# Kernel tuning notes

Hardware: AMD Instinct MI355X
Metric: run time of the kernel (lower is better)

## Reference

```python
import jax, jax.numpy as jnp
import numpy as np

D_MODEL = 512
D_INNER = 1024   # expand * d_model
D_STATE = 16
D_CONV = 4
DT_RANK = 32     # ceil(d_model / 16)
N_LAYERS = 4
N_PRED_LAYERS = 2
FEAT = 128
LN_EPS = 1e-5


def _ln(x, w, b):
    m = x.mean(-1, keepdims=True)
    v = ((x - m) ** 2).mean(-1, keepdims=True)
    return (x - m) * jax.lax.rsqrt(v + LN_EPS) * w + b


def _silu(x):
    return x * jax.nn.sigmoid(x)


def _causal_conv(x, w, b):
    # depthwise causal conv1d: x (B,L,C), w (C,K), b (C,)
    K = w.shape[1]
    L = x.shape[1]
    xp = jnp.pad(x, ((0, 0), (K - 1, 0), (0, 0)))
    y = b
    for k in range(K):
        y = y + xp[:, k:k + L, :] * w[:, k]
    return y


def _mamba(x, in_w, conv_w, conv_b, xp_w, dt_w, dt_b, Alog, Dp, out_w):
    # x: (B,L,d_model)
    xz = jnp.einsum('bld,ed->ble', x, in_w)          # (B,L,2*d_inner)
    xi, z = jnp.split(xz, 2, axis=-1)
    xc = _silu(_causal_conv(xi, conv_w, conv_b))     # (B,L,d_inner)
    dbc = jnp.einsum('blc,ec->ble', xc, xp_w)        # (B,L,dt_rank+2N)
    dt = dbc[..., :DT_RANK]
    Bm = dbc[..., DT_RANK:DT_RANK + D_STATE]         # (B,L,N)
    Cm = dbc[..., DT_RANK + D_STATE:]                # (B,L,N)
    delta = jax.nn.softplus(jnp.einsum('blr,cr->blc', dt, dt_w) + dt_b)  # (B,L,d_inner)
    A = -jnp.exp(Alog)                               # (d_inner,N), negative
    dA = jnp.exp(delta[..., None] * A)               # (B,L,d_inner,N)
    dBu = delta[..., None] * Bm[:, :, None, :] * xc[..., None]

    def step(h, inp):
        dA_t, dBu_t, C_t = inp
        h = dA_t * h + dBu_t                         # (B,d_inner,N)
        y = jnp.einsum('bcn,bn->bc', h, C_t)
        return h, y

    h0 = jnp.zeros((x.shape[0], D_INNER, D_STATE), x.dtype)
    _, ys = jax.lax.scan(step, h0, (dA.transpose(1, 0, 2, 3),
                                    dBu.transpose(1, 0, 2, 3),
                                    Cm.transpose(1, 0, 2)))
    y = ys.transpose(1, 0, 2) + Dp * xc              # skip connection D*u
    y = y * _silu(z)
    return jnp.einsum('blc,dc->bld', y, out_w)


def _forward(x, inp_w, inp_b, enc_ln_w, enc_ln_b, enc_in_w, enc_conv_w, enc_conv_b,
             enc_xp_w, enc_dt_w, enc_dt_b, enc_Alog, enc_D, enc_out_w,
             fin_ln_w, fin_ln_b, prd_ln_w, prd_ln_b, prd_in_w, prd_conv_w, prd_conv_b,
             prd_xp_w, prd_dt_w, prd_dt_b, prd_Alog, prd_D, prd_out_w,
             prd_nrm_w, prd_nrm_b, prd_proj_w, prd_proj_b):
    # MambaEncoder: input_proj + n_layers pre-norm residual Mamba blocks + final LN
    h = jnp.einsum('blf,df->bld', x, inp_w) + inp_b
    for i in range(N_LAYERS):
        h = h + _mamba(_ln(h, enc_ln_w[i], enc_ln_b[i]),
                       enc_in_w[i], enc_conv_w[i], enc_conv_b[i], enc_xp_w[i],
                       enc_dt_w[i], enc_dt_b[i], enc_Alog[i], enc_D[i], enc_out_w[i])
    ctx = _ln(h, fin_ln_w, fin_ln_b)
    # MambaPredictor: small causal mamba stack + norm + proj
    p = ctx
    for i in range(N_PRED_LAYERS):
        p = p + _mamba(_ln(p, prd_ln_w[i], prd_ln_b[i]),
                       prd_in_w[i], prd_conv_w[i], prd_conv_b[i], prd_xp_w[i],
                       prd_dt_w[i], prd_dt_b[i], prd_Alog[i], prd_D[i], prd_out_w[i])
    p = _ln(p, prd_nrm_w, prd_nrm_b)
    preds = jnp.einsum('bld,ed->ble', p, prd_proj_w) + prd_proj_b
    return preds


def _mamba_params(key, n, scale=0.02):
    ks = jax.random.split(key, 6)
    arange_A = jnp.tile(jnp.log(jnp.arange(1, D_STATE + 1, dtype=jnp.float32)), (n, D_INNER, 1))
    return dict(
        in_w=jax.random.normal(ks[0], (n, 2 * D_INNER, D_MODEL)) * scale,
        conv_w=jax.random.normal(ks[1], (n, D_INNER, D_CONV)) * scale,
        conv_b=jnp.zeros((n, D_INNER)),
        xp_w=jax.random.normal(ks[2], (n, DT_RANK + 2 * D_STATE, D_INNER)) * scale,
        dt_w=jax.random.normal(ks[3], (n, D_INNER, DT_RANK)) * scale,
        dt_b=jnp.full((n, D_INNER), jnp.log(jnp.expm1(0.01))),  # inv-softplus(0.01)
        Alog=arange_A,
        D=jnp.ones((n, D_INNER)),
        out_w=jax.random.normal(ks[4], (n, D_MODEL, D_INNER)) * scale,
    )


def setup_inputs() -> dict:
    key = jax.random.key(0)
    ks = jax.random.split(key, 8)
    enc = _mamba_params(ks[0], N_LAYERS)
    prd = _mamba_params(ks[1], N_PRED_LAYERS)
    return {
        'x': jax.random.normal(ks[2], (2, 1024, FEAT), dtype=jnp.float32),
        'inp_w': jax.random.normal(ks[3], (D_MODEL, FEAT)) * 0.02,
        'inp_b': jnp.zeros((D_MODEL,)),
        'enc_ln_w': jnp.ones((N_LAYERS, D_MODEL)), 'enc_ln_b': jnp.zeros((N_LAYERS, D_MODEL)),
        'enc_in_w': enc['in_w'], 'enc_conv_w': enc['conv_w'], 'enc_conv_b': enc['conv_b'],
        'enc_xp_w': enc['xp_w'], 'enc_dt_w': enc['dt_w'], 'enc_dt_b': enc['dt_b'],
        'enc_Alog': enc['Alog'], 'enc_D': enc['D'], 'enc_out_w': enc['out_w'],
        'fin_ln_w': jnp.ones((D_MODEL,)), 'fin_ln_b': jnp.zeros((D_MODEL,)),
        'prd_ln_w': jnp.ones((N_PRED_LAYERS, D_MODEL)), 'prd_ln_b': jnp.zeros((N_PRED_LAYERS, D_MODEL)),
        'prd_in_w': prd['in_w'], 'prd_conv_w': prd['conv_w'], 'prd_conv_b': prd['conv_b'],
        'prd_xp_w': prd['xp_w'], 'prd_dt_w': prd['dt_w'], 'prd_dt_b': prd['dt_b'],
        'prd_Alog': prd['Alog'], 'prd_D': prd['D'], 'prd_out_w': prd['out_w'],
        'prd_nrm_w': jnp.ones((D_MODEL,)), 'prd_nrm_b': jnp.zeros((D_MODEL,)),
        'prd_proj_w': jax.random.normal(ks[4], (D_MODEL, D_MODEL)) * 0.02,
        'prd_proj_b': jnp.zeros((D_MODEL,)),
    }


def reference(x, inp_w, inp_b, enc_ln_w, enc_ln_b, enc_in_w, enc_conv_w, enc_conv_b,
              enc_xp_w, enc_dt_w, enc_dt_b, enc_Alog, enc_D, enc_out_w,
              fin_ln_w, fin_ln_b, prd_ln_w, prd_ln_b, prd_in_w, prd_conv_w, prd_conv_b,
              prd_xp_w, prd_dt_w, prd_dt_b, prd_Alog, prd_D, prd_out_w,
              prd_nrm_w, prd_nrm_b, prd_proj_w, prd_proj_b):
    return _forward(x, inp_w, inp_b, enc_ln_w, enc_ln_b, enc_in_w, enc_conv_w, enc_conv_b,
                    enc_xp_w, enc_dt_w, enc_dt_b, enc_Alog, enc_D, enc_out_w,
                    fin_ln_w, fin_ln_b, prd_ln_w, prd_ln_b, prd_in_w, prd_conv_w, prd_conv_b,
                    prd_xp_w, prd_dt_w, prd_dt_b, prd_Alog, prd_D, prd_out_w,
                    prd_nrm_w, prd_nrm_b, prd_proj_w, prd_proj_b)
```

## Files before the change

kernel.cpp:

```cpp
#include <hip/hip_runtime.h>
#include <hip/hip_bf16.h>

using bf16 = __hip_bfloat16;
typedef __attribute__((ext_vector_type(8))) short short8;
typedef __attribute__((ext_vector_type(4))) float f32x4;

static constexpr int LB = 2;
static constexpr int LL = 1024;
static constexpr int DM = 512;
static constexpr int DI = 1024;
static constexpr int DSN = 16;
static constexpr int RK = 32;
static constexpr int MR_ROWS = LB * LL;

static constexpr int NCHUNK = 64;
static constexpr int CH = LL / NCHUNK;

__device__ __forceinline__ void gload16(const void* g, void* l) {
    __builtin_amdgcn_global_load_lds(
        (__attribute__((address_space(1))) void*)(g),
        (__attribute__((address_space(3))) void*)(l), 16, 0, 0);
}

struct ConvArgs {
    const float* src[9];
    bf16*        dst[9];
    int          n4[9];
};

__global__ __launch_bounds__(256) void convert_bf16_multi(ConvArgs a) {
    const int s = blockIdx.y;
    const float4* __restrict__ src = (const float4*)a.src[s];
    bf16* __restrict__ dst = a.dst[s];
    const int n4 = a.n4[s];
    for (int i = blockIdx.x * 256 + threadIdx.x; i < n4; i += gridDim.x * 256) {
        float4 v = src[i];
        bf16 t[4] = {__float2bfloat16(v.x), __float2bfloat16(v.y),
                     __float2bfloat16(v.z), __float2bfloat16(v.w)};
        *(uint2*)(dst + (size_t)i * 4) = *(uint2*)t;
    }
}

__global__ __launch_bounds__(256) void transpose_dtw(const float* __restrict__ enc_dtw,
                                                     const float* __restrict__ prd_dtw,
                                                     float* __restrict__ out) {
    const int layer = blockIdx.y;
    const float* src = (layer < 4) ? enc_dtw + (size_t)layer * DI * RK
                                   : prd_dtw + (size_t)(layer - 4) * DI * RK;
    float* dst = out + (size_t)layer * RK * DI;
    const int idx = blockIdx.x * 256 + threadIdx.x;
    const int k = idx >> 10, c = idx & (DI - 1);
    dst[idx] = src[(size_t)c * RK + k];
}

__device__ __forceinline__ void ln_store8(float* outrow, int lane,
                                          const float* v) {
    float4 a = {v[0], v[1], v[2], v[3]}, b = {v[4], v[5], v[6], v[7]};
    ((float4*)outrow)[lane] = a;
    ((float4*)outrow)[lane + 64] = b;
}
__device__ __forceinline__ void ln_store8(bf16* outrow, int lane,
                                          const float* v) {
    bf16 t0[4] = {__float2bfloat16(v[0]), __float2bfloat16(v[1]),
                  __float2bfloat16(v[2]), __float2bfloat16(v[3])};
    bf16 t1[4] = {__float2bfloat16(v[4]), __float2bfloat16(v[5]),
                  __float2bfloat16(v[6]), __float2bfloat16(v[7])};
    ((uint2*)outrow)[lane] = *(uint2*)t0;
    ((uint2*)outrow)[lane + 64] = *(uint2*)t1;
}

template <typename T>
__global__ __launch_bounds__(256) void ln_kernel(const float* __restrict__ x,
                                                 const float* __restrict__ w,
                                                 const float* __restrict__ b,
                                                 T* __restrict__ out,
                                                 float* __restrict__ dbc_zero) {
    if (dbc_zero != nullptr && blockIdx.x < 128) {
        ((float4*)dbc_zero)[blockIdx.x * 256 + threadIdx.x] =
            make_float4(0.f, 0.f, 0.f, 0.f);
    }
    const int wid = threadIdx.x >> 6, lane = threadIdx.x & 63;
    const int row = blockIdx.x * 4 + wid;
    const float4* xr = (const float4*)(x + (size_t)row * DM);
    const float4 v0 = xr[lane], v1 = xr[lane + 64];

    float s = (v0.x + v0.y + v0.z + v0.w) + (v1.x + v1.y + v1.z + v1.w);
#pragma unroll
    for (int m = 1; m < 64; m <<= 1) s += __shfl_xor(s, m);
    const float mean = s * (1.f / DM);

    float d[8] = {v0.x - mean, v0.y - mean, v0.z - mean, v0.w - mean,
                  v1.x - mean, v1.y - mean, v1.z - mean, v1.w - mean};
    float s2 = 0.f;
#pragma unroll
    for (int q = 0; q < 8; ++q) s2 += d[q] * d[q];
#pragma unroll
    for (int m = 1; m < 64; m <<= 1) s2 += __shfl_xor(s2, m);
    const float rs = rsqrtf(s2 * (1.f / DM) + 1e-5f);

    const float4 w0 = ((const float4*)w)[lane], w1 = ((const float4*)w)[lane + 64];
    const float4 b0 = ((const float4*)b)[lane], b1 = ((const float4*)b)[lane + 64];
    float o[8] = {d[0] * rs * w0.x + b0.x, d[1] * rs * w0.y + b0.y,
                  d[2] * rs * w0.z + b0.z, d[3] * rs * w0.w + b0.w,
                  d[4] * rs * w1.x + b1.x, d[5] * rs * w1.y + b1.y,
                  d[6] * rs * w1.z + b1.z, d[7] * rs * w1.w + b1.w};
    ln_store8(out + (size_t)row * DM, lane, o);
}

template <int BM, int BN, int BK, int EPI>
__global__ __launch_bounds__(256) void gemm_bt(const bf16* __restrict__ A, int lda,
                                               const bf16* __restrict__ B, int ldb,
                                               float* __restrict__ C, int ldc,
                                               int K, const float* __restrict__ bias) {
    static_assert(BK == 64, "layout assumes 128B LDS row");
    static_assert(BM % 32 == 0 && BN % 32 == 0, "wave staging granularity");
    constexpr int MR = (BM / 2) / 16;
    constexpr int NR = (BN / 2) / 16;
    __shared__ __align__(16) char sA[BM * 128];
    __shared__ __align__(16) char sB[BN * 128];

    const int tid = threadIdx.x;
    const int lane = tid & 63, wid = tid >> 6;
    const int wr = wid >> 1, wc = wid & 1;
    const int m0 = blockIdx.y * BM, n0 = blockIdx.x * BN;
    const int kbase = (EPI == 2) ? blockIdx.z * K : 0;

    f32x4 acc[MR][NR] = {};

    const int lrow = lane >> 3;
    const int lcol = (lane & 7) ^ lrow;
    const size_t lda2 = (size_t)lda * 2, ldb2 = (size_t)ldb * 2;
    const char* Ab = (const char*)A + (size_t)(m0 + wid * (BM / 4) + lrow) * lda2
                     + lcol * 16 + (size_t)kbase * 2;
    const char* Bb = (const char*)B + (size_t)(n0 + wid * (BN / 4) + lrow) * ldb2
                     + lcol * 16 + (size_t)kbase * 2;
    char* sAw = sA + wid * (BM / 4) * 128;
    char* sBw = sB + wid * (BN / 4) * 128;

    for (int k0 = 0; k0 < K; k0 += BK) {
#pragma unroll
        for (int i = 0; i < BM / 32; ++i)
            gload16(Ab + (size_t)i * 8 * lda2 + (size_t)k0 * 2, sAw + i * 1024);
#pragma unroll
        for (int i = 0; i < BN / 32; ++i)
            gload16(Bb + (size_t)i * 8 * ldb2 + (size_t)k0 * 2, sBw + i * 1024);
        __syncthreads();
#pragma unroll
        for (int kk = 0; kk < BK; kk += 32) {
            const int kb2 = (kk + (lane >> 4) * 8) * 2;
            short8 af[MR], bfr[NR];
#pragma unroll
            for (int m = 0; m < MR; ++m) {
                const int r = wr * (BM / 2) + m * 16 + (lane & 15);
                af[m] = *(const short8*)(sA + r * 128 + (kb2 ^ ((r & 7) << 4)));
            }
#pragma unroll
            for (int n = 0; n < NR; ++n) {
                const int r = wc * (BN / 2) + n * 16 + (lane & 15);
                bfr[n] = *(const short8*)(sB + r * 128 + (kb2 ^ ((r & 7) << 4)));
            }
#pragma unroll
            for (int m = 0; m < MR; ++m) {
#pragma unroll
                for (int n = 0; n < NR; ++n) {
                    acc[m][n] = __builtin_amdgcn_mfma_f32_16x16x32_bf16(af[m], bfr[n], acc[m][n], 0, 0, 0);
                }
            }
        }
        __syncthreads();
    }

#pragma unroll
    for (int m = 0; m < MR; ++m) {
#pragma unroll
        for (int n = 0; n < NR; ++n) {
            const int col = n0 + wc * (BN / 2) + n * 16 + (lane & 15);
            const float bv = (EPI == 1) ? bias[col] : 0.f;
#pragma unroll
            for (int j = 0; j < 4; ++j) {
                const int row = m0 + wr * (BM / 2) + m * 16 + (lane >> 4) * 4 + j;
                float v = acc[m][n][j] + bv;
                if (EPI == 4) {
                    ((bf16*)C)[(size_t)row * ldc + col] = __float2bfloat16(v);
                } else {
                    float* p = C + (size_t)row * ldc + col;
                    if (EPI == 2) {
                        atomicAdd(p, v);
                    } else {
                        if (EPI == 3) v += *p;
                        *p = v;
                    }
                }
            }
        }
    }
}

__global__ __launch_bounds__(256) void conv_mfma(const bf16* __restrict__ xzb,
                                                 const float* __restrict__ cw,
                                                 const float* __restrict__ cb,
                                                 const bf16* __restrict__ xpw,
                                                 bf16* __restrict__ xc_bf,
                                                 float* __restrict__ dbc) {
    const int c0 = blockIdx.x * 64;
    const int r0 = blockIdx.y * 64;
    const int tid = threadIdx.x, lane = tid & 63, wid = tid >> 6;
    __shared__ __align__(16) char sX[64 * 128];
    __shared__ __align__(16) char sW[64 * 128];

    const int lrow = lane >> 3, lcol = (lane & 7) ^ lrow;
    {
        const char* Wb = (const char*)xpw + (size_t)(wid * 16 + lrow) * (DI * 2)
                         + c0 * 2 + lcol * 16;
        char* sWw = sW + wid * 16 * 128;
        gload16(Wb, sWw);
        gload16(Wb + 8 * (DI * 2), sWw + 8 * 128);
    }

    const int c = lane;
    const int rgrp = wid;
    const float4 w = *(const float4*)(cw + (size_t)(c0 + c) * 4);
    const float cbv = cb[c0 + c];
#pragma unroll
    for (int i = 0; i < 16; ++i) {
        const int r = rgrp + i * 4;
        const int rowg = r0 + r;
        const int bstart = (rowg >> 10) << 10;
        const bf16* xi = xzb + (size_t)rowg * (2 * DI) + c0 + c;
        float acc = cbv + w.w * __bfloat162float(xi[0]);
        if (rowg - 1 >= bstart) acc += w.z * __bfloat162float(xi[-(2 * DI)]);
        if (rowg - 2 >= bstart) acc += w.y * __bfloat162float(xi[-(4 * DI)]);
        if (rowg - 3 >= bstart) acc += w.x * __bfloat162float(xi[-(6 * DI)]);
        const float s = acc / (1.f + expf(-acc));
        const bf16 sb = __float2bfloat16(s);
        xc_bf[(size_t)rowg * DI + c0 + c] = sb;
        *(bf16*)(sX + r * 128 + ((c * 2) ^ ((r & 7) << 4))) = sb;
    }
    __syncthreads();

    f32x4 acc[4] = {};
    const int kb2 = (lane >> 4) * 16;
#pragma unroll
    for (int kk = 0; kk < 2; ++kk) {
        const int kbyte = kk * 64 + kb2;
        const int ra = wid * 16 + (lane & 15);
        const short8 af = *(const short8*)(sX + ra * 128 + (kbyte ^ ((ra & 7) << 4)));
#pragma unroll
        for (int n = 0; n < 4; ++n) {
            const int re = n * 16 + (lane & 15);
            const short8 bfr = *(const short8*)(sW + re * 128 + (kbyte ^ ((re & 7) << 4)));
            acc[n] = __builtin_amdgcn_mfma_f32_16x16x32_bf16(af, bfr, acc[n], 0, 0, 0);
        }
    }
#pragma unroll
    for (int n = 0; n < 4; ++n) {
        const int col = n * 16 + (lane & 15);
#pragma unroll
        for (int j = 0; j < 4; ++j) {
            const int row = r0 + wid * 16 + (lane >> 4) * 4 + j;
            atomicAdd(&dbc[(size_t)row * 64 + col], acc[n][j]);
        }
    }
}

__global__ __launch_bounds__(256) void scan_part1(const bf16* __restrict__ xcb,
                                                  const float* __restrict__ dbc,
                                                  const float* __restrict__ Alog,
                                                  const float* __restrict__ dtw_t,
                                                  const float* __restrict__ dtb,
                                                  float* __restrict__ psum,
                                                  float* __restrict__ ssum) {
    const int lane = threadIdx.x & 63;
    const int wsub = threadIdx.x >> 6;
    const int c = blockIdx.x * 64 + lane;
    const int chunk = blockIdx.y * 4 + wsub;
    const int b = blockIdx.z;
    const int r0 = b * LL + chunk * CH;

    float wv[RK];
#pragma unroll
    for (int k = 0; k < RK; ++k) wv[k] = dtw_t[(size_t)k * DI + c];
    const float bdt = dtb[c];

    float a2[DSN];
#pragma unroll
    for (int q = 0; q < 4; ++q) {
        const float4 al = *(const float4*)(Alog + (size_t)c * DSN + q * 4);
        a2[q * 4 + 0] = -expf(al.x) * 1.44269504f;
        a2[q * 4 + 1] = -expf(al.y) * 1.44269504f;
        a2[q * 4 + 2] = -expf(al.z) * 1.44269504f;
        a2[q * 4 + 3] = -expf(al.w) * 1.44269504f;
    }

    float h[DSN], P[DSN];
#pragma unroll
    for (int n = 0; n < DSN; ++n) { h[n] = 0.f; P[n] = 1.f; }

    for (int t = 0; t < CH; ++t) {
        const size_t r = r0 + t;
        float acc = bdt;
#pragma unroll
        for (int q = 0; q < RK / 4; ++q) {
            const float4 d4 = *(const float4*)(dbc + r * 64 + q * 4);
            acc = fmaf(d4.x, wv[q * 4 + 0], acc);
            acc = fmaf(d4.y, wv[q * 4 + 1], acc);
            acc = fmaf(d4.z, wv[q * 4 + 2], acc);
            acc = fmaf(d4.w, wv[q * 4 + 3], acc);
        }
        const float d = (acc > 20.f) ? acc : log1pf(expf(acc));

        const float xv = __bfloat162float(xcb[r * DI + c]);
        const float dxv = d * xv;
        float Bv[DSN];
#pragma unroll
        for (int q = 0; q < 4; ++q)
            *(float4*)&Bv[q * 4] = *(const float4*)(dbc + r * 64 + 32 + q * 4);
#pragma unroll
        for (int n = 0; n < DSN; ++n) {
            const float dA = exp2f(d * a2[n]);
            h[n] = fmaf(dA, h[n], dxv * Bv[n]);
            P[n] *= dA;
        }
    }

    const size_t obase = ((size_t)(b * NCHUNK + chunk) * DSN) * DI + c;
#pragma unroll
    for (int n = 0; n < DSN; ++n) {
        psum[obase + (size_t)n * DI] = P[n];
        ssum[obase + (size_t)n * DI] = h[n];
    }
}

__global__ __launch_bounds__(256) void scan_combine(float* __restrict__ psum,
                                                    const float* __restrict__ ssum) {
    const int lane = threadIdx.x & 63;
    const int idx = blockIdx.y * 4 + (threadIdx.x >> 6);
    const int b = idx >> 4, n = idx & 15;
    const int c = blockIdx.x * 64 + lane;
    const size_t base = ((size_t)(b * NCHUNK) * DSN + n) * DI + c;
    const size_t stride = (size_t)DSN * DI;

    float h = 0.f;
    for (int j0 = 0; j0 < NCHUNK; j0 += 8) {
        float Pv[8], Sv[8];
#pragma unroll
        for (int u = 0; u < 8; ++u) {
            Pv[u] = psum[base + (j0 + u) * stride];
            Sv[u] = ssum[base + (j0 + u) * stride];
        }
#pragma unroll
        for (int u = 0; u < 8; ++u) {
            psum[base + (j0 + u) * stride] = h;
            h = fmaf(Pv[u], h, Sv[u]);
        }
    }
}

__global__ __launch_bounds__(256) void scan_part3(const bf16* __restrict__ xcb,
                                                  const bf16* __restrict__ xzb,
                                                  const float* __restrict__ dbc,
                                                  const float* __restrict__ Alog,
                                                  const float* __restrict__ dtw_t,
                                                  const float* __restrict__ dtb,
                                                  const float* __restrict__ Dp,
                                                  const float* __restrict__ hin,
                                                  bf16* __restrict__ yg) {
    const int lane = threadIdx.x & 63;
    const int wsub = threadIdx.x >> 6;
    const int c = blockIdx.x * 64 + lane;
    const int chunk = blockIdx.y * 4 + wsub;
    const int b = blockIdx.z;
    const int r0 = b * LL + chunk * CH;

    float wv[RK];
#pragma unroll
    for (int k = 0; k < RK; ++k) wv[k] = dtw_t[(size_t)k * DI + c];
    const float bdt = dtb[c];

    float a2[DSN];
#pragma unroll
    for (int q = 0; q < 4; ++q) {
        const float4 al = *(const float4*)(Alog + (size_t)c * DSN + q * 4);
        a2[q * 4 + 0] = -expf(al.x) * 1.44269504f;
        a2[q * 4 + 1] = -expf(al.y) * 1.44269504f;
        a2[q * 4 + 2] = -expf(al.z) * 1.44269504f;
        a2[q * 4 + 3] = -expf(al.w) * 1.44269504f;
    }
    const float dp = Dp[c];

    float h[DSN];
    const size_t hbase = ((size_t)(b * NCHUNK + chunk) * DSN) * DI + c;
#pragma unroll
    for (int n = 0; n < DSN; ++n) h[n] = hin[hbase + (size_t)n * DI];

    for (int t = 0; t < CH; ++t) {
        const size_t r = r0 + t;
        float acc = bdt;
#pragma unroll
        for (int q = 0; q < RK / 4; ++q) {
            const float4 d4 = *(const float4*)(dbc + r * 64 + q * 4);
            acc = fmaf(d4.x, wv[q * 4 + 0], acc);
            acc = fmaf(d4.y, wv[q * 4 + 1], acc);
            acc = fmaf(d4.z, wv[q * 4 + 2], acc);
            acc = fmaf(d4.w, wv[q * 4 + 3], acc);
        }
        const float d = (acc > 20.f) ? acc : log1pf(expf(acc));

        const float xv = __bfloat162float(xcb[r * DI + c]);
        const float zv = __bfloat162float(xzb[r * (2 * DI) + DI + c]);
        const float dxv = d * xv;
        float Bv[DSN], Cv[DSN];
#pragma unroll
        for (int q = 0; q < 4; ++q) {
            *(float4*)&Bv[q * 4] = *(const float4*)(dbc + r * 64 + 32 + q * 4);
            *(float4*)&Cv[q * 4] = *(const float4*)(dbc + r * 64 + 48 + q * 4);
        }
        float y0 = 0.f, y1 = 0.f, y2 = 0.f, y3 = 0.f;
#pragma unroll
        for (int q = 0; q < 4; ++q) {
            {
                const float dA = exp2f(d * a2[q * 4 + 0]);
                h[q * 4 + 0] = fmaf(dA, h[q * 4 + 0], dxv * Bv[q * 4 + 0]);
                y0 = fmaf(h[q * 4 + 0], Cv[q * 4 + 0], y0);
            }
            {
                const float dA = exp2f(d * a2[q * 4 + 1]);
                h[q * 4 + 1] = fmaf(dA, h[q * 4 + 1], dxv * Bv[q * 4 + 1]);
                y1 = fmaf(h[q * 4 + 1], Cv[q * 4 + 1], y1);
            }
            {
                const float dA = exp2f(d * a2[q * 4 + 2]);
                h[q * 4 + 2] = fmaf(dA, h[q * 4 + 2], dxv * Bv[q * 4 + 2]);
                y2 = fmaf(h[q * 4 + 2], Cv[q * 4 + 2], y2);
            }
            {
                const float dA = exp2f(d * a2[q * 4 + 3]);
                h[q * 4 + 3] = fmaf(dA, h[q * 4 + 3], dxv * Bv[q * 4 + 3]);
                y3 = fmaf(h[q * 4 + 3], Cv[q * 4 + 3], y3);
            }
        }
        const float y = (y0 + y1) + (y2 + y3);
        const float zs = zv / (1.f + expf(-zv));
        yg[r * DI + c] = __float2bfloat16((y + dp * xv) * zs);
    }
}

static void run_mamba_layer(hipStream_t stream, float* resid,
                            const float* ln_w, const float* ln_b,
                            const bf16* inw_bf,
                            const float* conv_w, const float* conv_b,
                            const bf16* xpw_bf,
                            const float* dtw_t, const float* dt_b,
                            const float* Alog, const float* Dp,
                            const bf16* outw_bf,
                            bf16* ln_bf, bf16* xzb, bf16* xc_bf,
                            float* dbc,
                            float* psum, float* ssum, bf16* yg_bf) {
    ln_kernel<bf16><<<MR_ROWS / 4, 256, 0, stream>>>(resid, ln_w, ln_b, ln_bf, dbc);
    gemm_bt<64, 64, 64, 4><<<dim3(2 * DI / 64, MR_ROWS / 64), 256, 0, stream>>>(
        ln_bf, DM, inw_bf, DM, (float*)xzb, 2 * DI, DM, nullptr);
    conv_mfma<<<dim3(DI / 64, MR_ROWS / 64), 256, 0, stream>>>(
        xzb, conv_w, conv_b, xpw_bf, xc_bf, dbc);
    scan_part1<<<dim3(DI / 64, NCHUNK / 4, LB), 256, 0, stream>>>(
        xc_bf, dbc, Alog, dtw_t, dt_b, psum, ssum);
    scan_combine<<<dim3(DI / 64, (LB * DSN) / 4), 256, 0, stream>>>(psum, ssum);
    scan_part3<<<dim3(DI / 64, NCHUNK / 4, LB), 256, 0, stream>>>(
        xc_bf, xzb, dbc, Alog, dtw_t, dt_b, Dp, psum, yg_bf);
    gemm_bt<32, 64, 64, 3><<<dim3(DM / 64, MR_ROWS / 32), 256, 0, stream>>>(
        yg_bf, DI, outw_bf, DI, resid, DM, DI, nullptr);
}

extern "C" void kernel_launch(void* const* d_in, const int* in_sizes, int n_in,
                              void* d_out, int out_size, void* d_ws, size_t ws_size,
                              hipStream_t stream) {
    const float* x         = (const float*)d_in[0];
    const float* inp_w     = (const float*)d_in[1];
    const float* inp_b     = (const float*)d_in[2];
    const float* enc_ln_w  = (const float*)d_in[3];
    const float* enc_ln_b  = (const float*)d_in[4];
    const float* enc_in_w  = (const float*)d_in[5];
    const float* enc_conv_w= (const float*)d_in[6];
    const float* enc_conv_b= (const float*)d_in[7];
    const float* enc_xp_w  = (const float*)d_in[8];
    const float* enc_dt_w  = (const float*)d_in[9];
    const float* enc_dt_b  = (const float*)d_in[10];
    const float* enc_Alog  = (const float*)d_in[11];
    const float* enc_D     = (const float*)d_in[12];
    const float* enc_out_w = (const float*)d_in[13];
    const float* fin_ln_w  = (const float*)d_in[14];
    const float* fin_ln_b  = (const float*)d_in[15];
    const float* prd_ln_w  = (const float*)d_in[16];
    const float* prd_ln_b  = (const float*)d_in[17];
    const float* prd_in_w  = (const float*)d_in[18];
    const float* prd_conv_w= (const float*)d_in[19];
    const float* prd_conv_b= (const float*)d_in[20];
    const float* prd_xp_w  = (const float*)d_in[21];
    const float* prd_dt_w  = (const float*)d_in[22];
    const float* prd_dt_b  = (const float*)d_in[23];
    const float* prd_Alog  = (const float*)d_in[24];
    const float* prd_D     = (const float*)d_in[25];
    const float* prd_out_w = (const float*)d_in[26];
    const float* prd_nrm_w = (const float*)d_in[27];
    const float* prd_nrm_b = (const float*)d_in[28];
    const float* prd_proj_w= (const float*)d_in[29];
    const float* prd_proj_b= (const float*)d_in[30];

    char* wp = (char*)d_ws;
    auto carve = [&](size_t elems, size_t esz) {
        void* p = (void*)wp;
        wp += (elems * esz + 255) & ~(size_t)255;
        return p;
    };
    bf16* x_bf     = (bf16*)carve((size_t)MR_ROWS * 128, 2);
    bf16* inpw_bf  = (bf16*)carve((size_t)DM * 128, 2);
    bf16* einw_bf  = (bf16*)carve(4ull * 2 * DI * DM, 2);
    bf16* expw_bf  = (bf16*)carve(4ull * 64 * DI, 2);
    bf16* eoutw_bf = (bf16*)carve(4ull * DM * DI, 2);
    bf16* pinw_bf  = (bf16*)carve(2ull * 2 * DI * DM, 2);
    bf16* pxpw_bf  = (bf16*)carve(2ull * 64 * DI, 2);
    bf16* poutw_bf = (bf16*)carve(2ull * DM * DI, 2);
    bf16* projw_bf = (bf16*)carve((size_t)DM * DM, 2);
    float* dtwt    = (float*)carve(6ull * RK * DI, 4);
    float* hbuf    = (float*)carve((size_t)MR_ROWS * DM, 4);
    float* pbuf    = (float*)carve((size_t)MR_ROWS * DM, 4);
    bf16* ln_bf    = (bf16*)carve((size_t)MR_ROWS * DM, 2);
    bf16* xzb      = (bf16*)carve((size_t)MR_ROWS * 2 * DI, 2);
    bf16* xc_bf    = (bf16*)carve((size_t)MR_ROWS * DI, 2);
    float* dbc     = (float*)carve((size_t)MR_ROWS * 64, 4);
    float* psum    = (float*)carve((size_t)LB * NCHUNK * DSN * DI, 4);
    float* ssum    = (float*)carve((size_t)LB * NCHUNK * DSN * DI, 4);
    bf16* yg_bf    = (bf16*)carve((size_t)MR_ROWS * DI, 2);

    ConvArgs ca;
    const float* csrc[9] = {x, inp_w, enc_in_w, enc_xp_w, enc_out_w,
                            prd_in_w, prd_xp_w, prd_out_w, prd_proj_w};
    bf16* cdst[9] = {x_bf, inpw_bf, einw_bf, expw_bf, eoutw_bf,
                     pinw_bf, pxpw_bf, poutw_bf, projw_bf};
    const int cn[9] = {MR_ROWS * 128, DM * 128, 4 * 2 * DI * DM, 4 * 64 * DI, 4 * DM * DI,
                       2 * 2 * DI * DM, 2 * 64 * DI, 2 * DM * DI, DM * DM};
    for (int i = 0; i < 9; ++i) { ca.src[i] = csrc[i]; ca.dst[i] = cdst[i]; ca.n4[i] = cn[i] / 4; }
    convert_bf16_multi<<<dim3(128, 9), 256, 0, stream>>>(ca);
    transpose_dtw<<<dim3(RK * DI / 256, 6), 256, 0, stream>>>(enc_dt_w, prd_dt_w, dtwt);

    gemm_bt<32, 64, 64, 1><<<dim3(DM / 64, MR_ROWS / 32), 256, 0, stream>>>(
        x_bf, 128, inpw_bf, 128, hbuf, DM, 128, inp_b);

    for (int i = 0; i < 4; ++i) {
        run_mamba_layer(stream, hbuf,
                        enc_ln_w + (size_t)i * DM, enc_ln_b + (size_t)i * DM,
                        einw_bf + (size_t)i * 2 * DI * DM,
                        enc_conv_w + (size_t)i * DI * 4, enc_conv_b + (size_t)i * DI,
                        expw_bf + (size_t)i * 64 * DI,
                        dtwt + (size_t)i * RK * DI, enc_dt_b + (size_t)i * DI,
                        enc_Alog + (size_t)i * DI * DSN, enc_D + (size_t)i * DI,
                        eoutw_bf + (size_t)i * DM * DI,
                        ln_bf, xzb, xc_bf, dbc, psum, ssum, yg_bf);
    }

    ln_kernel<float><<<MR_ROWS / 4, 256, 0, stream>>>(hbuf, fin_ln_w, fin_ln_b, pbuf, nullptr);

    for (int i = 0; i < 2; ++i) {
        run_mamba_layer(stream, pbuf,
                        prd_ln_w + (size_t)i * DM, prd_ln_b + (size_t)i * DM,
                        pinw_bf + (size_t)i * 2 * DI * DM,
                        prd_conv_w + (size_t)i * DI * 4, prd_conv_b + (size_t)i * DI,
                        pxpw_bf + (size_t)i * 64 * DI,
                        dtwt + (size_t)(4 + i) * RK * DI, prd_dt_b + (size_t)i * DI,
                        prd_Alog + (size_t)i * DI * DSN, prd_D + (size_t)i * DI,
                        poutw_bf + (size_t)i * DM * DI,
                        ln_bf, xzb, xc_bf, dbc, psum, ssum, yg_bf);
    }

    ln_kernel<bf16><<<MR_ROWS / 4, 256, 0, stream>>>(pbuf, prd_nrm_w, prd_nrm_b, ln_bf, nullptr);
    gemm_bt<32, 64, 64, 1><<<dim3(DM / 64, MR_ROWS / 32), 256, 0, stream>>>(
        ln_bf, DM, projw_bf, DM, (float*)d_out, DM, DM, prd_proj_b);

    (void)in_sizes; (void)n_in; (void)out_size; (void)ws_size;
}
```

Measured before the change: 693.7 us.

## Fuse LayerNorm into in-proj GEMM and split conv from x-proj GEMM

Adds a new ln_gemm kernel that computes LayerNorm row statistics and normalizes fp32 activations directly into the LDS A-tile. This removes the separate LN kernel and the bf16 LN buffer, both for the Mamba in-projection and for the final projection. The fused conv+MFMA x-projection kernel is replaced by an elementwise conv+SiLU kernel followed by a split-K gemm_bt that accumulates into dbc with atomics. The cost is that LN is recomputed in every column block, so the fp32 activations are reread many times. Variance is now taken as E[x^2]-mean^2, which is less numerically precise.

```diff
diff --git a/kernel.cpp b/kernel.cpp
--- a/kernel.cpp
+++ b/kernel.cpp
@@ -53,32 +53,10 @@
     dst[idx] = src[(size_t)c * RK + k];
 }
 
-__device__ __forceinline__ void ln_store8(float* outrow, int lane,
-                                          const float* v) {
-    float4 a = {v[0], v[1], v[2], v[3]}, b = {v[4], v[5], v[6], v[7]};
-    ((float4*)outrow)[lane] = a;
-    ((float4*)outrow)[lane + 64] = b;
-}
-__device__ __forceinline__ void ln_store8(bf16* outrow, int lane,
-                                          const float* v) {
-    bf16 t0[4] = {__float2bfloat16(v[0]), __float2bfloat16(v[1]),
-                  __float2bfloat16(v[2]), __float2bfloat16(v[3])};
-    bf16 t1[4] = {__float2bfloat16(v[4]), __float2bfloat16(v[5]),
-                  __float2bfloat16(v[6]), __float2bfloat16(v[7])};
-    ((uint2*)outrow)[lane] = *(uint2*)t0;
-    ((uint2*)outrow)[lane + 64] = *(uint2*)t1;
-}
-
-template <typename T>
 __global__ __launch_bounds__(256) void ln_kernel(const float* __restrict__ x,
                                                  const float* __restrict__ w,
                                                  const float* __restrict__ b,
-                                                 T* __restrict__ out,
-                                                 float* __restrict__ dbc_zero) {
-    if (dbc_zero != nullptr && blockIdx.x < 128) {
-        ((float4*)dbc_zero)[blockIdx.x * 256 + threadIdx.x] =
-            make_float4(0.f, 0.f, 0.f, 0.f);
-    }
+                                                 float* __restrict__ out) {
     const int wid = threadIdx.x >> 6, lane = threadIdx.x & 63;
     const int row = blockIdx.x * 4 + wid;
     const float4* xr = (const float4*)(x + (size_t)row * DM);
@@ -100,11 +78,12 @@
 
     const float4 w0 = ((const float4*)w)[lane], w1 = ((const float4*)w)[lane + 64];
     const float4 b0 = ((const float4*)b)[lane], b1 = ((const float4*)b)[lane + 64];
-    float o[8] = {d[0] * rs * w0.x + b0.x, d[1] * rs * w0.y + b0.y,
-                  d[2] * rs * w0.z + b0.z, d[3] * rs * w0.w + b0.w,
-                  d[4] * rs * w1.x + b1.x, d[5] * rs * w1.y + b1.y,
-                  d[6] * rs * w1.z + b1.z, d[7] * rs * w1.w + b1.w};
-    ln_store8(out + (size_t)row * DM, lane, o);
+    float4 o0 = {d[0] * rs * w0.x + b0.x, d[1] * rs * w0.y + b0.y,
+                 d[2] * rs * w0.z + b0.z, d[3] * rs * w0.w + b0.w};
+    float4 o1 = {d[4] * rs * w1.x + b1.x, d[5] * rs * w1.y + b1.y,
+                 d[6] * rs * w1.z + b1.z, d[7] * rs * w1.w + b1.w};
+    ((float4*)(out + (size_t)row * DM))[lane] = o0;
+    ((float4*)(out + (size_t)row * DM))[lane + 64] = o1;
 }
 
 template <int BM, int BN, int BK, int EPI>
@@ -180,87 +159,150 @@
             for (int j = 0; j < 4; ++j) {
                 const int row = m0 + wr * (BM / 2) + m * 16 + (lane >> 4) * 4 + j;
                 float v = acc[m][n][j] + bv;
+                float* p = C + (size_t)row * ldc + col;
+                if (EPI == 2) {
+                    atomicAdd(p, v);
+                } else {
+                    if (EPI == 3) v += *p;
+                    *p = v;
+                }
+            }
+        }
+    }
+}
+
+template <int BN, int EPI>
+__global__ __launch_bounds__(256) void ln_gemm(const float* __restrict__ A,
+                                               const float* __restrict__ lnw,
+                                               const float* __restrict__ lnb,
+                                               const bf16* __restrict__ B,
+                                               float* __restrict__ C, int ldc,
+                                               const float* __restrict__ bias) {
+    constexpr int BM = 64, BK = 64;
+    constexpr int MR = 2;
+    constexpr int NR = (BN / 2) / 16;
+    __shared__ __align__(16) char sA[BM * 128];
+    __shared__ __align__(16) char sB[BN * 128];
+
+    const int tid = threadIdx.x;
+    const int lane = tid & 63, wid = tid >> 6;
+    const int wr = wid >> 1, wc = wid & 1;
+    const int m0 = blockIdx.y * BM, n0 = blockIdx.x * BN;
+    const int rloc = tid >> 2, q = tid & 3;
+
+    const float* Arow = A + (size_t)(m0 + rloc) * DM;
+    float s = 0.f, s2 = 0.f;
+#pragma unroll
+    for (int i = 0; i < 32; ++i) {
+        const float4 v = ((const float4*)Arow)[q * 32 + i];
+        s += (v.x + v.y) + (v.z + v.w);
+        s2 += (v.x * v.x + v.y * v.y) + (v.z * v.z + v.w * v.w);
+    }
+    s += __shfl_xor(s, 1);  s += __shfl_xor(s, 2);
+    s2 += __shfl_xor(s2, 1); s2 += __shfl_xor(s2, 2);
+    const float mean = s * (1.f / DM);
+    const float rs = rsqrtf(s2 * (1.f / DM) - mean * mean + 1e-5f);
+
+    const int lrow = lane >> 3, lcol = (lane & 7) ^ lrow;
+    const char* Bb = (const char*)B + (size_t)(n0 + wid * (BN / 4) + lrow) * (DM * 2)
+                     + lcol * 16;
+    char* sBw = sB + wid * (BN / 4) * 128;
+
+    f32x4 acc[MR][NR] = {};
+
+    for (int k0 = 0; k0 < DM; k0 += BK) {
+#pragma unroll
+        for (int g = 0; g < 2; ++g) {
+            const int cb = k0 + g * 32 + q * 8;
+            const float4 xa = *(const float4*)(Arow + cb);
+            const float4 xb = *(const float4*)(Arow + cb + 4);
+            const float4 wa = *(const float4*)(lnw + cb);
+            const float4 wb = *(const float4*)(lnw + cb + 4);
+            const float4 ba = *(const float4*)(lnb + cb);
+            const float4 bb = *(const float4*)(lnb + cb + 4);
+            bf16 t[8] = {
+                __float2bfloat16((xa.x - mean) * rs * wa.x + ba.x),
+                __float2bfloat16((xa.y - mean) * rs * wa.y + ba.y),
+                __float2bfloat16((xa.z - mean) * rs * wa.z + ba.z),
+                __float2bfloat16((xa.w - mean) * rs * wa.w + ba.w),
+                __float2bfloat16((xb.x - mean) * rs * wb.x + bb.x),
+                __float2bfloat16((xb.y - mean) * rs * wb.y + bb.y),
+                __float2bfloat16((xb.z - mean) * rs * wb.z + bb.z),
+                __float2bfloat16((xb.w - mean) * rs * wb.w + bb.w)};
+            const int blk = g * 4 + q;
+            const int swz = blk ^ (rloc & 7);
+            *(short8*)(sA + rloc * 128 + swz * 16) = *(short8*)t;
+        }
+#pragma unroll
+        for (int i = 0; i < BN / 32; ++i)
+            gload16(Bb + (size_t)i * 8 * (DM * 2) + (size_t)k0 * 2, sBw + i * 1024);
+        __syncthreads();
+#pragma unroll
+        for (int kk = 0; kk < BK; kk += 32) {
+            const int kb2 = (kk + (lane >> 4) * 8) * 2;
+            short8 af[MR], bfr[NR];
+#pragma unroll
+            for (int m = 0; m < MR; ++m) {
+                const int r = wr * 32 + m * 16 + (lane & 15);
+                af[m] = *(const short8*)(sA + r * 128 + (kb2 ^ ((r & 7) << 4)));
+            }
+#pragma unroll
+            for (int n = 0; n < NR; ++n) {
+                const int r = wc * (BN / 2) + n * 16 + (lane & 15);
+                bfr[n] = *(const short8*)(sB + r * 128 + (kb2 ^ ((r & 7) << 4)));
+            }
+#pragma unroll
+            for (int m = 0; m < MR; ++m) {
+#pragma unroll
+                for (int n = 0; n < NR; ++n) {
+                    acc[m][n] = __builtin_amdgcn_mfma_f32_16x16x32_bf16(af[m], bfr[n], acc[m][n], 0, 0, 0);
+                }
+            }
+        }
+        __syncthreads();
+    }
+
+#pragma unroll
+    for (int m = 0; m < MR; ++m) {
+#pragma unroll
+        for (int n = 0; n < NR; ++n) {
+            const int col = n0 + wc * (BN / 2) + n * 16 + (lane & 15);
+            const float bv = (EPI == 1) ? bias[col] : 0.f;
+#pragma unroll
+            for (int j = 0; j < 4; ++j) {
+                const int row = m0 + wr * 32 + m * 16 + (lane >> 4) * 4 + j;
+                const float v = acc[m][n][j] + bv;
                 if (EPI == 4) {
                     ((bf16*)C)[(size_t)row * ldc + col] = __float2bfloat16(v);
                 } else {
-                    float* p = C + (size_t)row * ldc + col;
-                    if (EPI == 2) {
-                        atomicAdd(p, v);
-                    } else {
-                        if (EPI == 3) v += *p;
-                        *p = v;
-                    }
+                    C[(size_t)row * ldc + col] = v;
                 }
             }
         }
     }
 }
 
-__global__ __launch_bounds__(256) void conv_mfma(const bf16* __restrict__ xzb,
-                                                 const float* __restrict__ cw,
-                                                 const float* __restrict__ cb,
-                                                 const bf16* __restrict__ xpw,
-                                                 bf16* __restrict__ xc_bf,
-                                                 float* __restrict__ dbc) {
-    const int c0 = blockIdx.x * 64;
-    const int r0 = blockIdx.y * 64;
-    const int tid = threadIdx.x, lane = tid & 63, wid = tid >> 6;
-    __shared__ __align__(16) char sX[64 * 128];
-    __shared__ __align__(16) char sW[64 * 128];
-
-    const int lrow = lane >> 3, lcol = (lane & 7) ^ lrow;
-    {
-        const char* Wb = (const char*)xpw + (size_t)(wid * 16 + lrow) * (DI * 2)
-                         + c0 * 2 + lcol * 16;
-        char* sWw = sW + wid * 16 * 128;
-        gload16(Wb, sWw);
-        gload16(Wb + 8 * (DI * 2), sWw + 8 * 128);
-    }
-
-    const int c = lane;
-    const int rgrp = wid;
-    const float4 w = *(const float4*)(cw + (size_t)(c0 + c) * 4);
-    const float cbv = cb[c0 + c];
-#pragma unroll
-    for (int i = 0; i < 16; ++i) {
-        const int r = rgrp + i * 4;
-        const int rowg = r0 + r;
-        const int bstart = (rowg >> 10) << 10;
-        const bf16* xi = xzb + (size_t)rowg * (2 * DI) + c0 + c;
-        float acc = cbv + w.w * __bfloat162float(xi[0]);
-        if (rowg - 1 >= bstart) acc += w.z * __bfloat162float(xi[-(2 * DI)]);
-        if (rowg - 2 >= bstart) acc += w.y * __bfloat162float(xi[-(4 * DI)]);
-        if (rowg - 3 >= bstart) acc += w.x * __bfloat162float(xi[-(6 * DI)]);
-        const float s = acc / (1.f + expf(-acc));
-        const bf16 sb = __float2bfloat16(s);
-        xc_bf[(size_t)rowg * DI + c0 + c] = sb;
-        *(bf16*)(sX + r * 128 + ((c * 2) ^ ((r & 7) << 4))) = sb;
-    }
-    __syncthreads();
-
-    f32x4 acc[4] = {};
-    const int kb2 = (lane >> 4) * 16;
-#pragma unroll
-    for (int kk = 0; kk < 2; ++kk) {
-        const int kbyte = kk * 64 + kb2;
-        const int ra = wid * 16 + (lane & 15);
-        const short8 af = *(const short8*)(sX + ra * 128 + (kbyte ^ ((ra & 7) << 4)));
-#pragma unroll
-        for (int n = 0; n < 4; ++n) {
-            const int re = n * 16 + (lane & 15);
-            const short8 bfr = *(const short8*)(sW + re * 128 + (kbyte ^ ((re & 7) << 4)));
-            acc[n] = __builtin_amdgcn_mfma_f32_16x16x32_bf16(af, bfr, acc[n], 0, 0, 0);
-        }
-    }
-#pragma unroll
-    for (int n = 0; n < 4; ++n) {
-        const int col = n * 16 + (lane & 15);
-#pragma unroll
-        for (int j = 0; j < 4; ++j) {
-            const int row = r0 + wid * 16 + (lane >> 4) * 4 + j;
-            atomicAdd(&dbc[(size_t)row * 64 + col], acc[n][j]);
-        }
-    }
+__global__ __launch_bounds__(256) void conv_silu_b(const bf16* __restrict__ xzb,
+                                                   const float* __restrict__ cw,
+                                                   const float* __restrict__ cb,
+                                                   bf16* __restrict__ xc_bf,
+                                                   float* __restrict__ dbc_zero) {
+    if (blockIdx.x < 128) {
+        ((float4*)dbc_zero)[blockIdx.x * 256 + threadIdx.x] =
+            make_float4(0.f, 0.f, 0.f, 0.f);
+    }
+    const int idx = blockIdx.x * 256 + threadIdx.x;
+    const int c = idx & (DI - 1);
+    const int r = idx >> 10;
+    const int l = r & (LL - 1);
+    const bf16* xi = xzb + (size_t)r * (2 * DI) + c;
+    const float4 w = *(const float4*)(cw + (size_t)c * 4);
+    float acc = cb[c] + w.w * __bfloat162float(xi[0]);
+    if (l >= 1) acc += w.z * __bfloat162float(xi[-(2 * DI)]);
+    if (l >= 2) acc += w.y * __bfloat162float(xi[-(4 * DI)]);
+    if (l >= 3) acc += w.x * __bfloat162float(xi[-(6 * DI)]);
+    const float s = acc / (1.f + expf(-acc));
+    xc_bf[idx] = __float2bfloat16(s);
 }
 
 __global__ __launch_bounds__(256) void scan_part1(const bf16* __restrict__ xcb,
@@ -453,14 +495,13 @@
                             const float* dtw_t, const float* dt_b,
                             const float* Alog, const float* Dp,
                             const bf16* outw_bf,
-                            bf16* ln_bf, bf16* xzb, bf16* xc_bf,
-                            float* dbc,
+                            bf16* xzb, bf16* xc_bf, float* dbc,
                             float* psum, float* ssum, bf16* yg_bf) {
-    ln_kernel<bf16><<<MR_ROWS / 4, 256, 0, stream>>>(resid, ln_w, ln_b, ln_bf, dbc);
-    gemm_bt<64, 64, 64, 4><<<dim3(2 * DI / 64, MR_ROWS / 64), 256, 0, stream>>>(
-        ln_bf, DM, inw_bf, DM, (float*)xzb, 2 * DI, DM, nullptr);
-    conv_mfma<<<dim3(DI / 64, MR_ROWS / 64), 256, 0, stream>>>(
-        xzb, conv_w, conv_b, xpw_bf, xc_bf, dbc);
+    ln_gemm<64, 4><<<dim3(2 * DI / 64, MR_ROWS / 64), 256, 0, stream>>>(
+        resid, ln_w, ln_b, inw_bf, (float*)xzb, 2 * DI, nullptr);
+    conv_silu_b<<<MR_ROWS * DI / 256, 256, 0, stream>>>(xzb, conv_w, conv_b, xc_bf, dbc);
+    gemm_bt<32, 64, 64, 2><<<dim3(1, MR_ROWS / 32, 4), 256, 0, stream>>>(
+        xc_bf, DI, xpw_bf, DI, dbc, 64, DI / 4, nullptr);
     scan_part1<<<dim3(DI / 64, NCHUNK / 4, LB), 256, 0, stream>>>(
         xc_bf, dbc, Alog, dtw_t, dt_b, psum, ssum);
     scan_combine<<<dim3(DI / 64, (LB * DSN) / 4), 256, 0, stream>>>(psum, ssum);
@@ -523,7 +564,6 @@
     float* dtwt    = (float*)carve(6ull * RK * DI, 4);
     float* hbuf    = (float*)carve((size_t)MR_ROWS * DM, 4);
     float* pbuf    = (float*)carve((size_t)MR_ROWS * DM, 4);
-    bf16* ln_bf    = (bf16*)carve((size_t)MR_ROWS * DM, 2);
     bf16* xzb      = (bf16*)carve((size_t)MR_ROWS * 2 * DI, 2);
     bf16* xc_bf    = (bf16*)carve((size_t)MR_ROWS * DI, 2);
     float* dbc     = (float*)carve((size_t)MR_ROWS * 64, 4);
@@ -554,10 +594,10 @@
                         dtwt + (size_t)i * RK * DI, enc_dt_b + (size_t)i * DI,
                         enc_Alog + (size_t)i * DI * DSN, enc_D + (size_t)i * DI,
                         eoutw_bf + (size_t)i * DM * DI,
-                        ln_bf, xzb, xc_bf, dbc, psum, ssum, yg_bf);
-    }
-
-    ln_kernel<float><<<MR_ROWS / 4, 256, 0, stream>>>(hbuf, fin_ln_w, fin_ln_b, pbuf, nullptr);
+                        xzb, xc_bf, dbc, psum, ssum, yg_bf);
+    }
+
+    ln_kernel<<<MR_ROWS / 4, 256, 0, stream>>>(hbuf, fin_ln_w, fin_ln_b, pbuf);
 
     for (int i = 0; i < 2; ++i) {
         run_mamba_layer(stream, pbuf,
@@ -568,12 +608,11 @@
                         dtwt + (size_t)(4 + i) * RK * DI, prd_dt_b + (size_t)i * DI,
                         prd_Alog + (size_t)i * DI * DSN, prd_D + (size_t)i * DI,
                         poutw_bf + (size_t)i * DM * DI,
-                        ln_bf, xzb, xc_bf, dbc, psum, ssum, yg_bf);
-    }
-
-    ln_kernel<bf16><<<MR_ROWS / 4, 256, 0, stream>>>(pbuf, prd_nrm_w, prd_nrm_b, ln_bf, nullptr);
-    gemm_bt<32, 64, 64, 1><<<dim3(DM / 64, MR_ROWS / 32), 256, 0, stream>>>(
-        ln_bf, DM, projw_bf, DM, (float*)d_out, DM, DM, prd_proj_b);
+                        xzb, xc_bf, dbc, psum, ssum, yg_bf);
+    }
+
+    ln_gemm<64, 1><<<dim3(DM / 64, MR_ROWS / 64), 256, 0, stream>>>(
+        pbuf, prd_nrm_w, prd_nrm_b, projw_bf, (float*)d_out, DM, prd_proj_b);
 
     (void)in_sizes; (void)n_in; (void)out_size; (void)ws_size;
 }
```

Result: slower. 820.4 us (+18.3%).
